# Kernel tuning notes

Measured on AMD Instinct MI355X. Metric: run time of the kernel, lower is better.

The kernel has to match this reference:

```python
import jax, jax.numpy as jnp
import numpy as np

B, T, N, H = 16, 49, 64, 128  # batch, input_window_size-1, nbones, hidden_size


def setup_inputs() -> dict:
    key = jax.random.key(0)
    ks = jax.random.split(key, 13)
    s = 0.1  # keep gate preactivations in a sane range
    inp = {
        "h": jax.random.normal(ks[0], (B, T, N, H), jnp.float32),
        "c_h": jax.random.normal(ks[1], (B, T, N, H), jnp.float32),
        "p": jax.random.normal(ks[2], (B, T, N, H), jnp.float32),
        "g_t": jax.random.normal(ks[3], (B, T, 1, H), jnp.float32),
        "c_g_t": jax.random.normal(ks[4], (B, T, 1, H), jnp.float32),
        # 8 h-update gates stacked: order = (i, f_lt, f_ft, f_rt, f_s, g, o, c)
        "U": jax.random.normal(ks[5], (8, T, H, H), jnp.float32) * s,     # acts on p
        "Wt": jax.random.normal(ks[6], (8, T, 3 * H, H), jnp.float32) * s,  # acts on [h_before,h,h_after]
        "Ws": jax.random.normal(ks[7], (8, T, H, H), jnp.float32) * s,    # acts on h_s_before
        "Zt": jax.random.normal(ks[8], (8, T, H, H), jnp.float32) * s,    # acts on g_t
        "b": jax.random.normal(ks[9], (8, T, 1, H), jnp.float32) * s,
        # 3 g_t-update gates stacked: order = (forget_f, g, o)
        "Wg": jax.random.normal(ks[10], (3, T, H, H), jnp.float32) * s,
        "Zg": jax.random.normal(ks[11], (3, T, H, H), jnp.float32) * s,
        "bg": jax.random.normal(ks[12], (3, T, 1, H), jnp.float32) * s,
        "train": 0,
    }
    return inp


def _forward(h, c_h, p, g_t, c_g_t, U, Wt, Ws, Zt, b, Wg, Zg, bg):
    zt = jnp.zeros_like(h[:, :1])        # temporal padding [B,1,N,H]
    zs = jnp.zeros_like(h[:, :, :1])     # spatial  padding [B,T,1,H]
    h_tb = jnp.concatenate([zt, h[:, :-1]], axis=1)
    h_ta = jnp.concatenate([h[:, 1:], zt], axis=1)
    h_tba = jnp.concatenate([h_tb, h, h_ta], axis=3)   # [B,T,N,3H]
    c_tb = jnp.concatenate([zt, c_h[:, :-1]], axis=1)
    c_ta = jnp.concatenate([c_h[:, 1:], zt], axis=1)
    h_sb = jnp.concatenate([zs, h[:, :, :-1]], axis=2)
    c_sb = jnp.concatenate([zs, c_h[:, :, :-1]], axis=2)

    # all 8 gate preactivations at once; per-timestep weights contracted with einsum
    pre = (jnp.einsum('btnh,gthk->gbtnk', p, U)
           + jnp.einsum('btnd,gtdk->gbtnk', h_tba, Wt)
           + jnp.einsum('btnh,gthk->gbtnk', h_sb, Ws)
           + jnp.einsum('btoh,gthk->gbtok', g_t, Zt)   # o == 1, broadcasts over bones
           + b[:, None])                               # [8,B,T,N,H]
    i_n, f_lt, f_ft, f_rt, f_s, g_n, o_n = jax.nn.sigmoid(pre[:7])
    c_n = jnp.tanh(pre[7])

    c_h_new = (i_n * c_n + f_lt * c_tb + f_ft * c_h + f_rt * c_ta
               + f_s * c_sb + g_n * c_g_t)
    h_new = o_n * jnp.tanh(c_h_new)

    # global (g_t) state update
    h_mean = jnp.mean(h_new, axis=2, keepdims=True)    # [B,T,1,H]
    f_gtf = jax.nn.sigmoid(jnp.einsum('btnh,thk->btnk', h_new, Wg[0])
                           + jnp.einsum('btoh,thk->btok', g_t, Zg[0]) + bg[0])
    g_gtg = jax.nn.sigmoid(jnp.einsum('btoh,thk->btok', h_mean, Wg[1])
                           + jnp.einsum('btoh,thk->btok', g_t, Zg[1]) + bg[1])
    o_gto = jax.nn.sigmoid(jnp.einsum('btoh,thk->btok', h_mean, Wg[2])
                           + jnp.einsum('btoh,thk->btok', g_t, Zg[2]) + bg[2])
    c_g_new = jnp.mean(f_gtf * c_h_new, axis=2, keepdims=True) + g_gtg * c_g_t
    g_new = jnp.tanh(c_g_new) * o_gto
    return h_new, c_h_new, g_new, c_g_new


def reference(h, c_h, p, g_t, c_g_t, U, Wt, Ws, Zt, b, Wg, Zg, bg, train):
    return _forward(h, c_h, p, g_t, c_g_t, U, Wt, Ws, Zt, b, Wg, Zg, bg)
```

## Files before the change

kernel.cpp:

```cpp
#include <hip/hip_runtime.h>
#include <hip/hip_bf16.h>

#define TD 49
#define BD 16
#define ND 64
#define HD 128

typedef float  f32x4  __attribute__((ext_vector_type(4)));
typedef __bf16 bf16x8 __attribute__((ext_vector_type(8)));
typedef __bf16 bf16x4 __attribute__((ext_vector_type(4)));

#define WP_OFF   0u
#define WP_ELEMS 38535168u
#define HB_OFF   38535168u
#define ACT_ELEMS 6422528u
#define PB_OFF   44957696u
#define GB_OFF   51380224u
#define GT_ELEMS 100352u
#define ZP_OFF   51480576u

#define OUT_H    0
#define OUT_CH   6422528
#define OUT_G    12845056
#define OUT_CG   12945408

#define KPAD 136
#define LDS1_BYTES 65536

__device__ __forceinline__ float sigf(float x) {
    return 1.0f / (1.0f + exp2f(-1.442695041f * x));
}
__device__ __forceinline__ float tanhf_fast(float x) {
    x = fminf(fmaxf(x, -20.f), 20.f);
    float e = exp2f(2.885390082f * x);
    return (e - 1.f) / (e + 1.f);
}
__device__ __forceinline__ void gload16(const void* g, void* l) {
    __builtin_amdgcn_global_load_lds((const __attribute__((address_space(1))) void*)g,
                                     (__attribute__((address_space(3))) void*)l, 16, 0, 0);
}

__global__ void prep_acts(const float* __restrict__ h, const float* __restrict__ p,
                          const float* __restrict__ g, __bf16* __restrict__ ws)
{
    unsigned i = blockIdx.x * 256u + threadIdx.x;
    const unsigned HU = ACT_ELEMS / 4u, GU = GT_ELEMS / 4u;
    const float* src;
    unsigned dst;
    if (i < HU)                 { src = h + (size_t)i * 4;          dst = HB_OFF + i * 4; }
    else if (i < 2u*HU)         { unsigned j = i - HU;   src = p + (size_t)j * 4; dst = PB_OFF + j * 4; }
    else if (i < 2u*HU + GU)    { unsigned j = i - 2u*HU; src = g + (size_t)j * 4; dst = GB_OFF + j * 4; }
    else if (i < 2u*HU + GU + 512u) {
        unsigned j = i - 2u*HU - GU;
        bf16x4 z = {};
        *(bf16x4*)(ws + ZP_OFF + j * 4) = z;
        return;
    } else return;
    f32x4 v = *(const f32x4*)src;
    bf16x4 w;
    w[0] = (__bf16)v[0]; w[1] = (__bf16)v[1]; w[2] = (__bf16)v[2]; w[3] = (__bf16)v[3];
    *(bf16x4*)(ws + dst) = w;
}

__global__ __launch_bounds__(256) void prep_w(
    const float* __restrict__ U, const float* __restrict__ Wt,
    const float* __restrict__ Ws, const float* __restrict__ Zt,
    __bf16* __restrict__ wp)
{
    __shared__ __bf16 tile[64 * 132];
    int bid = blockIdx.x;
    int tg  = bid / 12;
    int c   = bid % 12;
    int t   = tg >> 3, g = tg & 7;
    int gt  = g * TD + t;
    int tid = threadIdx.x;
    int k0  = c * 64;

#pragma unroll
    for (int u = 0; u < 8; ++u) {
        int unit = u * 256 + tid;
        int kk = unit >> 5;
        int h4 = (unit & 31) << 2;
        int k  = k0 + kk;
        const float* src;
        if (k < 128)      src = U  + ((size_t)(gt * 128 + k)       << 7);
        else if (k < 512) src = Wt + ((size_t)(gt * 384 + (k-128)) << 7);
        else if (k < 640) src = Ws + ((size_t)(gt * 128 + (k-512)) << 7);
        else              src = Zt + ((size_t)(gt * 128 + (k-640)) << 7);
        f32x4 v = *(const f32x4*)(src + h4);
        bf16x4 w;
        w[0] = (__bf16)v[0]; w[1] = (__bf16)v[1]; w[2] = (__bf16)v[2]; w[3] = (__bf16)v[3];
        *(bf16x4*)(tile + kk * 132 + h4) = w;
    }
    __syncthreads();
#pragma unroll
    for (int u = 0; u < 2; ++u) {
        int unit = u * 256 + tid;
        int hh = unit >> 2;
        int kg = unit & 3;
        bf16x8 v0, v1;
#pragma unroll
        for (int j = 0; j < 8; ++j) v0[j] = tile[(kg * 16 + j) * 132 + hh];
#pragma unroll
        for (int j = 0; j < 8; ++j) v1[j] = tile[(kg * 16 + 8 + j) * 132 + hh];
        __bf16* dst = wp + (size_t)(tg * 128 + hh) * 768 + k0 + kg * 16;
        *(bf16x8*)dst       = v0;
        *(bf16x8*)(dst + 8) = v1;
    }
}

__global__ __launch_bounds__(256, 2) void phase1_kernel(
    const __bf16* __restrict__ ws,
    const float* __restrict__ c_h, const float* __restrict__ c_g_t,
    const float* __restrict__ bias, float* __restrict__ out)
{
    extern __shared__ __bf16 smem[];
    const __bf16* hb = ws + HB_OFF;
    const __bf16* pb = ws + PB_OFF;
    const __bf16* gb = ws + GB_OFF;
    const __bf16* wp = ws + WP_OFF;
    const __bf16* zp = ws + ZP_OFF;

    int bid = blockIdx.x;
    int swz = (bid & 7) * 392 + (bid >> 3);
    int t     = swz >> 6;
    int rem   = swz & 63;
    int mtile = rem >> 3, ntile = rem & 7;

    int tid  = threadIdx.x;
    int wave = tid >> 6, lane = tid & 63;
    int lg = lane >> 4, l16 = lane & 15;

    const int ls   = lane >> 3;
    const int k16s = ((lane & 7) ^ ls) << 3;

    f32x4 acc[2][8];
    const f32x4 vzero = {0.f, 0.f, 0.f, 0.f};
#pragma unroll
    for (int mi = 0; mi < 2; ++mi)
#pragma unroll
        for (int g = 0; g < 8; ++g) acc[mi][g] = vzero;

    int rbA[2], rsA[2], rbB[8], rsB[8];
#pragma unroll
    for (int mi = 0; mi < 2; ++mi) {
        int row = wave * 32 + mi * 16 + l16;
        rbA[mi] = row << 7;
        rsA[mi] = (row & 7) << 4;
    }
#pragma unroll
    for (int g = 0; g < 8; ++g) {
        int row = g * 16 + l16;
        rbB[g] = row << 7;
        rsB[g] = (l16 & 7) << 4;
    }
    const int kb0 = lg << 4;

#define STAGE(BUF, KS) do {                                                     \
        int s_   = (KS) >> 1;                                                   \
        int koff = (((KS) & 1) << 6) + k16s;                                    \
        _Pragma("unroll")                                                       \
        for (int it = 0; it < 4; ++it) {                                        \
            int chunk = it * 4 + wave;                                          \
            int R   = chunk * 8 + ls;                                           \
            int b_  = mtile * 2 + (R >> 6);                                     \
            int n_  = R & 63;                                                   \
            int bt_ = b_ * TD + t;                                              \
            const __bf16* srcA;                                                 \
            if (s_ == 0)      srcA = pb + ((bt_ * ND + n_) << 7) + koff;        \
            else if (s_ == 1) srcA = (t > 0)    ? hb + (((bt_-1) * ND + n_) << 7) + koff : zp; \
            else if (s_ == 2) srcA = hb + ((bt_ * ND + n_) << 7) + koff;        \
            else if (s_ == 3) srcA = (t < TD-1) ? hb + (((bt_+1) * ND + n_) << 7) + koff : zp; \
            else if (s_ == 4) srcA = (n_ > 0)   ? hb + ((bt_ * ND + n_ - 1) << 7) + koff : zp; \
            else              srcA = gb + (bt_ << 7) + koff;                    \
            gload16(srcA, smem + (BUF) * 8192 + chunk * 512);                   \
            int g_ = R >> 4, hc = R & 15;                                       \
            const __bf16* srcB = wp + (size_t)((t * 8 + g_) * 128 + ntile * 16 + hc) * 768 \
                                    + ((KS) << 6) + k16s;                       \
            gload16(srcB, smem + 16384 + (BUF) * 8192 + chunk * 512);           \
        }                                                                       \
    } while (0)

    STAGE(0, 0);
    __syncthreads();

    int buf = 0;
    for (int ks = 0; ks < 12; ++ks) {
        if (ks < 11) STAGE(buf ^ 1, ks + 1);
        const char* Ab = (const char*)(smem + buf * 8192);
        const char* Bb = (const char*)(smem + 16384 + buf * 8192);
#pragma unroll
        for (int ks32 = 0; ks32 < 2; ++ks32) {
            bf16x8 af[2], bfr[8];
#pragma unroll
            for (int mi = 0; mi < 2; ++mi)
                af[mi] = *(const bf16x8*)(Ab + rbA[mi] + (((ks32 << 6) + kb0) ^ rsA[mi]));
#pragma unroll
            for (int g = 0; g < 8; ++g)
                bfr[g] = *(const bf16x8*)(Bb + rbB[g] + (((ks32 << 6) + kb0) ^ rsB[g]));
#pragma unroll
            for (int mi = 0; mi < 2; ++mi)
#pragma unroll
                for (int g = 0; g < 8; ++g)
                    acc[mi][g] = __builtin_amdgcn_mfma_f32_16x16x32_bf16(af[mi], bfr[g], acc[mi][g], 0, 0, 0);
        }
        __syncthreads();
        buf ^= 1;
    }

    const int hcol = ntile * 16 + l16;
    float bv[8];
#pragma unroll
    for (int g = 0; g < 8; ++g) bv[g] = bias[(g * TD + t) * HD + hcol];

#pragma unroll
    for (int mi = 0; mi < 2; ++mi) {
#pragma unroll
        for (int r = 0; r < 4; ++r) {
            int RG = mtile * 128 + wave * 32 + mi * 16 + lg * 4 + r;
            int b  = RG >> 6, nn = RG & 63;
            int bt = b * TD + t;
            int base = ((bt * ND + nn) << 7) + hcol;
            float pre[8];
#pragma unroll
            for (int g = 0; g < 8; ++g) pre[g] = acc[mi][g][r] + bv[g];
            float i_  = sigf(pre[0]);
            float flt = sigf(pre[1]);
            float fft = sigf(pre[2]);
            float frt = sigf(pre[3]);
            float fs  = sigf(pre[4]);
            float gn  = sigf(pre[5]);
            float on  = sigf(pre[6]);
            float cn  = tanhf_fast(pre[7]);
            float ccur = c_h[base];
            float ctb  = (t > 0)      ? c_h[base - ND * HD] : 0.f;
            float cta  = (t < TD - 1) ? c_h[base + ND * HD] : 0.f;
            float csb  = (nn > 0)     ? c_h[base - HD]      : 0.f;
            float cg   = c_g_t[(bt << 7) + hcol];
            float cnew = i_ * cn + flt * ctb + fft * ccur + frt * cta + fs * csb + gn * cg;
            float hnew = on * tanhf_fast(cnew);
            out[OUT_H  + base] = hnew;
            out[OUT_CH + base] = cnew;
        }
    }
#undef STAGE
}

__global__ __launch_bounds__(256, 2) void phase2_kernel(
    const float* __restrict__ g_t, const float* __restrict__ c_g_t,
    const float* __restrict__ Wg,  const float* __restrict__ Zg,
    const float* __restrict__ bg,  float* __restrict__ out)
{
    __shared__ __bf16 A2[64 * KPAD];
    __shared__ __bf16 Wb[128 * KPAD];
    __shared__ float  gts[128];
    __shared__ float  hm[128];
    __shared__ float  dots[5][128];
    __shared__ float  ps[2][128];
    __shared__ float  red[4][128];

    const int bid  = blockIdx.x;
    const int t    = bid >> 4;
    const int b    = bid & 15;
    const int tid  = threadIdx.x;
    const int wv   = tid >> 6;
    const int lane = tid & 63;
    const int lg   = lane >> 4;
    const int l16  = lane & 15;
    const int bt   = b * TD + t;

    const float* hn  = out + OUT_H;
    const float* chn = out + OUT_CH;

#pragma unroll
    for (int j = 0; j < 8; ++j) {
        int fid = j * 256 + tid;
        int r   = fid >> 5;
        int k   = (fid & 31) << 2;
        f32x4 v = *(const f32x4*)(hn + ((bt * ND + r) << 7) + k);
        bf16x4 w;
        w[0] = (__bf16)v[0]; w[1] = (__bf16)v[1]; w[2] = (__bf16)v[2]; w[3] = (__bf16)v[3];
        *(bf16x4*)(A2 + r * KPAD + k) = w;
    }
    if (tid < 128) gts[tid] = g_t[(bt << 7) + tid];
    __syncthreads();

    {
        int c = tid & 127, half = tid >> 7;
        float sum_ = 0.f;
        for (int r2 = 0; r2 < 32; ++r2) sum_ += (float)A2[(half * 32 + r2) * KPAD + c];
        ps[half][c] = sum_;
    }
    __syncthreads();
    if (tid < 128) hm[tid] = (ps[0][tid] + ps[1][tid]) * (1.f / 64.f);

    for (int m = 0; m < 5; ++m) {
        const float* M = (m < 3) ? (Zg + ((size_t)(m * TD + t) << 14))
                                 : (Wg + ((size_t)((m - 2) * TD + t) << 14));
        const bool use_hm = (m >= 3);
        __syncthreads();
#pragma unroll
        for (int j = 0; j < 16; ++j) {
            int fid = j * 256 + tid;
            int k   = fid >> 5;
            int c4  = (fid & 31) << 2;
            f32x4 v = *(const f32x4*)(M + (k << 7) + c4);
            bf16x4 w;
            w[0] = (__bf16)v[0]; w[1] = (__bf16)v[1]; w[2] = (__bf16)v[2]; w[3] = (__bf16)v[3];
            *(bf16x4*)(Wb + (k << 7) + c4) = w;
        }
        __syncthreads();
        {
            int c = tid & 127, half = tid >> 7;
            const float* vec = use_hm ? hm : gts;
            float sum_ = 0.f;
            for (int k = half * 64; k < half * 64 + 64; ++k)
                sum_ += vec[k] * (float)Wb[(k << 7) + c];
            ps[half][c] = sum_;
        }
        __syncthreads();
        if (tid < 128) dots[m][tid] = ps[0][tid] + ps[1][tid];
    }

    {
        const float* M = Wg + ((size_t)t << 14);
        __syncthreads();
#pragma unroll
        for (int j = 0; j < 16; ++j) {
            int fid = j * 256 + tid;
            int k   = fid >> 5;
            int q   = fid & 31;
            f32x4 v = *(const f32x4*)(M + (k << 7) + q * 4);
            int cb = q * 4;
            Wb[(cb + 0) * KPAD + k] = (__bf16)v[0];
            Wb[(cb + 1) * KPAD + k] = (__bf16)v[1];
            Wb[(cb + 2) * KPAD + k] = (__bf16)v[2];
            Wb[(cb + 3) * KPAD + k] = (__bf16)v[3];
        }
        __syncthreads();
    }

    f32x4 acc[8];
    const f32x4 vzero = {0.f, 0.f, 0.f, 0.f};
#pragma unroll
    for (int cf = 0; cf < 8; ++cf) acc[cf] = vzero;
#pragma unroll
    for (int ks = 0; ks < 4; ++ks) {
        int kb = ks * 32 + lg * 8;
        bf16x8 a = *(const bf16x8*)(A2 + (wv * 16 + l16) * KPAD + kb);
#pragma unroll
        for (int cf = 0; cf < 8; ++cf) {
            bf16x8 bfr = *(const bf16x8*)(Wb + (cf * 16 + l16) * KPAD + kb);
            acc[cf] = __builtin_amdgcn_mfma_f32_16x16x32_bf16(a, bfr, acc[cf], 0, 0, 0);
        }
    }

#pragma unroll
    for (int cf = 0; cf < 8; ++cf) {
        int col = cf * 16 + l16;
        float z = dots[0][col] + bg[(0 * TD + t) * HD + col];
        float macc = 0.f;
#pragma unroll
        for (int r = 0; r < 4; ++r) {
            int row = wv * 16 + lg * 4 + r;
            float f  = sigf(acc[cf][r] + z);
            float cv = chn[((bt * ND + row) << 7) + col];
            macc += f * cv;
        }
        macc += __shfl_xor(macc, 16, 64);
        macc += __shfl_xor(macc, 32, 64);
        if (lane < 16) red[wv][col] = macc;
    }
    __syncthreads();
    if (tid < 128) {
        int c = tid;
        float Mn  = (red[0][c] + red[1][c] + red[2][c] + red[3][c]) * (1.f / 64.f);
        float g_g = sigf(dots[3][c] + dots[1][c] + bg[(1 * TD + t) * HD + c]);
        float o_g = sigf(dots[4][c] + dots[2][c] + bg[(2 * TD + t) * HD + c]);
        float cgt = c_g_t[(bt << 7) + c];
        float cgn = Mn + g_g * cgt;
        float gnw = tanhf_fast(cgn) * o_g;
        out[OUT_G  + (bt << 7) + c] = gnw;
        out[OUT_CG + (bt << 7) + c] = cgn;
    }
}

extern "C" void kernel_launch(void* const* d_in, const int* in_sizes, int n_in,
                              void* d_out, int out_size, void* d_ws, size_t ws_size,
                              hipStream_t stream) {
    const float* h     = (const float*)d_in[0];
    const float* c_h   = (const float*)d_in[1];
    const float* p     = (const float*)d_in[2];
    const float* g_t   = (const float*)d_in[3];
    const float* c_g_t = (const float*)d_in[4];
    const float* U     = (const float*)d_in[5];
    const float* Wt    = (const float*)d_in[6];
    const float* Ws    = (const float*)d_in[7];
    const float* Zt    = (const float*)d_in[8];
    const float* b     = (const float*)d_in[9];
    const float* Wg    = (const float*)d_in[10];
    const float* Zg    = (const float*)d_in[11];
    const float* bg    = (const float*)d_in[12];
    float* out = (float*)d_out;
    __bf16* ws = (__bf16*)d_ws;

    prep_acts<<<12644, 256, 0, stream>>>(h, p, g_t, ws);
    prep_w<<<TD * 8 * 12, 256, 0, stream>>>(U, Wt, Ws, Zt, ws + WP_OFF);

    (void)hipFuncSetAttribute(reinterpret_cast<const void*>(phase1_kernel),
                              hipFuncAttributeMaxDynamicSharedMemorySize, LDS1_BYTES);
    phase1_kernel<<<TD * 64, 256, LDS1_BYTES, stream>>>(ws, c_h, c_g_t, b, out);
    phase2_kernel<<<TD * BD, 256, 0, stream>>>(g_t, c_g_t, Wg, Zg, bg, out);
}
```

Measured before the change: 253.3 us.

## Deepen phase1 GEMM pipeline to 4-stage ring and batch four batches per phase2 block

Phase1's K loop changes from a double-buffered 12-step loop over 128-wide K slices to a 24-step loop over 32-wide slices. It uses a 4-slot LDS ring with three slices in flight, precomputed source pointers and explicit vmcnt waits, so global-to-LDS loads overlap the MFMA work better. Phase2 now handles four batches per block (196 blocks instead of 784), so each Zg/Wg weight matrix is converted to bf16 and staged once per four batches instead of once per batch. The costs are more LDS per block, lower occupancy (launch bounds 1) and fewer blocks for the GPU to spread phase2 across.

Result: faster. 234.9 us (-7.3%).

```diff
diff --git a/kernel.cpp b/kernel.cpp
--- a/kernel.cpp
+++ b/kernel.cpp
@@ -11,7 +11,6 @@
 typedef __bf16 bf16x4 __attribute__((ext_vector_type(4)));
 
 #define WP_OFF   0u
-#define WP_ELEMS 38535168u
 #define HB_OFF   38535168u
 #define ACT_ELEMS 6422528u
 #define PB_OFF   44957696u
@@ -26,6 +25,7 @@
 
 #define KPAD 136
 #define LDS1_BYTES 65536
+#define LDS2_BYTES 118784
 
 __device__ __forceinline__ float sigf(float x) {
     return 1.0f / (1.0f + exp2f(-1.442695041f * x));
@@ -131,8 +131,39 @@
     int wave = tid >> 6, lane = tid & 63;
     int lg = lane >> 4, l16 = lane & 15;
 
-    const int ls   = lane >> 3;
-    const int k16s = ((lane & 7) ^ ls) << 3;
+    const __bf16* pA[2][6];
+    const __bf16* pB[2];
+    int dstA[2], dstB[2];
+#pragma unroll
+    for (int it = 0; it < 2; ++it) {
+        int chunk = it * 256 + tid;
+        int row   = chunk >> 2;
+        int k16   = chunk & 3;
+        int ke    = (k16 ^ ((row >> 1) & 3)) * 8;
+        int b_ = mtile * 2 + (row >> 6), n_ = row & 63, bt_ = b_ * TD + t;
+        pA[it][0] = pb + ((bt_ * ND + n_) << 7) + ke;
+        pA[it][1] = (t > 0)      ? hb + (((bt_ - 1) * ND + n_) << 7) + ke : zp + ke;
+        pA[it][2] = hb + ((bt_ * ND + n_) << 7) + ke;
+        pA[it][3] = (t < TD - 1) ? hb + (((bt_ + 1) * ND + n_) << 7) + ke : zp + ke;
+        pA[it][4] = (n_ > 0)     ? hb + ((bt_ * ND + n_ - 1) << 7) + ke : zp + ke;
+        pA[it][5] = gb + (bt_ << 7) + ke;
+        int g_ = row >> 4, hc = row & 15;
+        pB[it] = wp + (size_t)((t * 8 + g_) * 128 + ntile * 16 + hc) * 768 + ke;
+        dstA[it] = chunk * 8;
+        dstB[it] = 16384 + chunk * 8;
+    }
+
+    int rbA[2], rbB[8];
+#pragma unroll
+    for (int mi = 0; mi < 2; ++mi) {
+        int row = wave * 32 + mi * 16 + l16;
+        rbA[mi] = row * 64 + ((lg ^ ((row >> 1) & 3)) << 4);
+    }
+#pragma unroll
+    for (int g = 0; g < 8; ++g) {
+        int row = g * 16 + l16;
+        rbB[g] = 32768 + row * 64 + ((lg ^ ((row >> 1) & 3)) << 4);
+    }
 
     f32x4 acc[2][8];
     const f32x4 vzero = {0.f, 0.f, 0.f, 0.f};
@@ -141,72 +172,43 @@
 #pragma unroll
         for (int g = 0; g < 8; ++g) acc[mi][g] = vzero;
 
-    int rbA[2], rsA[2], rbB[8], rsB[8];
-#pragma unroll
-    for (int mi = 0; mi < 2; ++mi) {
-        int row = wave * 32 + mi * 16 + l16;
-        rbA[mi] = row << 7;
-        rsA[mi] = (row & 7) << 4;
-    }
-#pragma unroll
-    for (int g = 0; g < 8; ++g) {
-        int row = g * 16 + l16;
-        rbB[g] = row << 7;
-        rsB[g] = (l16 & 7) << 4;
-    }
-    const int kb0 = lg << 4;
-
-#define STAGE(BUF, KS) do {                                                     \
-        int s_   = (KS) >> 1;                                                   \
-        int koff = (((KS) & 1) << 6) + k16s;                                    \
+#define STAGE(KS) do {                                                          \
         _Pragma("unroll")                                                       \
-        for (int it = 0; it < 4; ++it) {                                        \
-            int chunk = it * 4 + wave;                                          \
-            int R   = chunk * 8 + ls;                                           \
-            int b_  = mtile * 2 + (R >> 6);                                     \
-            int n_  = R & 63;                                                   \
-            int bt_ = b_ * TD + t;                                              \
-            const __bf16* srcA;                                                 \
-            if (s_ == 0)      srcA = pb + ((bt_ * ND + n_) << 7) + koff;        \
-            else if (s_ == 1) srcA = (t > 0)    ? hb + (((bt_-1) * ND + n_) << 7) + koff : zp; \
-            else if (s_ == 2) srcA = hb + ((bt_ * ND + n_) << 7) + koff;        \
-            else if (s_ == 3) srcA = (t < TD-1) ? hb + (((bt_+1) * ND + n_) << 7) + koff : zp; \
-            else if (s_ == 4) srcA = (n_ > 0)   ? hb + ((bt_ * ND + n_ - 1) << 7) + koff : zp; \
-            else              srcA = gb + (bt_ << 7) + koff;                    \
-            gload16(srcA, smem + (BUF) * 8192 + chunk * 512);                   \
-            int g_ = R >> 4, hc = R & 15;                                       \
-            const __bf16* srcB = wp + (size_t)((t * 8 + g_) * 128 + ntile * 16 + hc) * 768 \
-                                    + ((KS) << 6) + k16s;                       \
-            gload16(srcB, smem + 16384 + (BUF) * 8192 + chunk * 512);           \
+        for (int it = 0; it < 2; ++it) {                                        \
+            gload16(pA[it][(KS) >> 2] + ((KS) & 3) * 32,                        \
+                    smem + ((KS) & 3) * 4096 + dstA[it]);                       \
+            gload16(pB[it] + (KS) * 32,                                         \
+                    smem + ((KS) & 3) * 4096 + dstB[it]);                       \
         }                                                                       \
     } while (0)
 
-    STAGE(0, 0);
-    __syncthreads();
-
-    int buf = 0;
-    for (int ks = 0; ks < 12; ++ks) {
-        if (ks < 11) STAGE(buf ^ 1, ks + 1);
-        const char* Ab = (const char*)(smem + buf * 8192);
-        const char* Bb = (const char*)(smem + 16384 + buf * 8192);
-#pragma unroll
-        for (int ks32 = 0; ks32 < 2; ++ks32) {
-            bf16x8 af[2], bfr[8];
-#pragma unroll
-            for (int mi = 0; mi < 2; ++mi)
-                af[mi] = *(const bf16x8*)(Ab + rbA[mi] + (((ks32 << 6) + kb0) ^ rsA[mi]));
-#pragma unroll
-            for (int g = 0; g < 8; ++g)
-                bfr[g] = *(const bf16x8*)(Bb + rbB[g] + (((ks32 << 6) + kb0) ^ rsB[g]));
-#pragma unroll
-            for (int mi = 0; mi < 2; ++mi)
-#pragma unroll
-                for (int g = 0; g < 8; ++g)
-                    acc[mi][g] = __builtin_amdgcn_mfma_f32_16x16x32_bf16(af[mi], bfr[g], acc[mi][g], 0, 0, 0);
-        }
-        __syncthreads();
-        buf ^= 1;
-    }
+    STAGE(0); STAGE(1); STAGE(2);
+    asm volatile("s_waitcnt vmcnt(8)" ::: "memory");
+    __builtin_amdgcn_s_barrier();
+
+#pragma unroll
+    for (int ks = 0; ks < 24; ++ks) {
+        if (ks + 3 < 24) STAGE(ks + 3);
+        const char* base = (const char*)smem + (ks & 3) * 8192;
+        bf16x8 af[2], bfr[8];
+        af[0] = *(const bf16x8*)(base + rbA[0]);
+        af[1] = *(const bf16x8*)(base + rbA[1]);
+#pragma unroll
+        for (int g = 0; g < 8; ++g)
+            bfr[g] = *(const bf16x8*)(base + rbB[g]);
+#pragma unroll
+        for (int g = 0; g < 8; ++g) {
+            acc[0][g] = __builtin_amdgcn_mfma_f32_16x16x32_bf16(af[0], bfr[g], acc[0][g], 0, 0, 0);
+            acc[1][g] = __builtin_amdgcn_mfma_f32_16x16x32_bf16(af[1], bfr[g], acc[1][g], 0, 0, 0);
+        }
+        if (ks < 23) {
+            if (ks < 21)       asm volatile("s_waitcnt vmcnt(8)" ::: "memory");
+            else if (ks == 21) asm volatile("s_waitcnt vmcnt(4)" ::: "memory");
+            else               asm volatile("s_waitcnt vmcnt(0)" ::: "memory");
+            __builtin_amdgcn_s_barrier();
+        }
+    }
+#undef STAGE
 
     const int hcol = ntile * 16 + l16;
     float bv[8];
@@ -243,93 +245,87 @@
             out[OUT_CH + base] = cnew;
         }
     }
-#undef STAGE
-}
-
-__global__ __launch_bounds__(256, 2) void phase2_kernel(
+}
+
+__global__ __launch_bounds__(256, 1) void phase2_kernel(
     const float* __restrict__ g_t, const float* __restrict__ c_g_t,
     const float* __restrict__ Wg,  const float* __restrict__ Zg,
     const float* __restrict__ bg,  float* __restrict__ out)
 {
-    __shared__ __bf16 A2[64 * KPAD];
-    __shared__ __bf16 Wb[128 * KPAD];
-    __shared__ float  gts[128];
-    __shared__ float  hm[128];
-    __shared__ float  dots[5][128];
-    __shared__ float  ps[2][128];
-    __shared__ float  red[4][128];
-
-    const int bid  = blockIdx.x;
-    const int t    = bid >> 4;
-    const int b    = bid & 15;
-    const int tid  = threadIdx.x;
-    const int wv   = tid >> 6;
-    const int lane = tid & 63;
-    const int lg   = lane >> 4;
-    const int l16  = lane & 15;
-    const int bt   = b * TD + t;
+    extern __shared__ char sm2[];
+    __bf16* A2  = (__bf16*)sm2;
+    __bf16* Wb  = (__bf16*)(sm2 + 69632);
+    float*  gts = (float*)(sm2 + 69632 + 34816);
+    float*  hm  = (float*)(sm2 + 69632 + 34816 + 2048);
+    float*  dts = (float*)(sm2 + 69632 + 34816 + 4096);
+
+    int bid = blockIdx.x;
+    int t = bid >> 2, bq = bid & 3;
+    int tid = threadIdx.x;
+    int wv = tid >> 6, lane = tid & 63, lg = lane >> 4, l16 = lane & 15;
 
     const float* hn  = out + OUT_H;
     const float* chn = out + OUT_CH;
 
 #pragma unroll
-    for (int j = 0; j < 8; ++j) {
+    for (int j = 0; j < 32; ++j) {
         int fid = j * 256 + tid;
-        int r   = fid >> 5;
-        int k   = (fid & 31) << 2;
-        f32x4 v = *(const f32x4*)(hn + ((bt * ND + r) << 7) + k);
+        int r = fid >> 5, k = (fid & 31) << 2;
+        int b = bq * 4 + (r >> 6), n = r & 63, bt = b * TD + t;
+        f32x4 v = *(const f32x4*)(hn + ((bt * ND + n) << 7) + k);
         bf16x4 w;
         w[0] = (__bf16)v[0]; w[1] = (__bf16)v[1]; w[2] = (__bf16)v[2]; w[3] = (__bf16)v[3];
         *(bf16x4*)(A2 + r * KPAD + k) = w;
     }
-    if (tid < 128) gts[tid] = g_t[(bt << 7) + tid];
+#pragma unroll
+    for (int j = 0; j < 2; ++j) {
+        int idx = j * 256 + tid;
+        int b4 = idx >> 7, c = idx & 127;
+        gts[idx] = g_t[(((bq * 4 + b4) * TD + t) << 7) + c];
+    }
     __syncthreads();
 
-    {
-        int c = tid & 127, half = tid >> 7;
-        float sum_ = 0.f;
-        for (int r2 = 0; r2 < 32; ++r2) sum_ += (float)A2[(half * 32 + r2) * KPAD + c];
-        ps[half][c] = sum_;
+#pragma unroll
+    for (int j = 0; j < 2; ++j) {
+        int idx = j * 256 + tid;
+        int b4 = idx >> 7, c = idx & 127;
+        float s = 0.f;
+        for (int n = 0; n < 64; ++n) s += (float)A2[(b4 * 64 + n) * KPAD + c];
+        hm[idx] = s * (1.f / 64.f);
     }
     __syncthreads();
-    if (tid < 128) hm[tid] = (ps[0][tid] + ps[1][tid]) * (1.f / 64.f);
 
     for (int m = 0; m < 5; ++m) {
         const float* M = (m < 3) ? (Zg + ((size_t)(m * TD + t) << 14))
                                  : (Wg + ((size_t)((m - 2) * TD + t) << 14));
-        const bool use_hm = (m >= 3);
-        __syncthreads();
 #pragma unroll
         for (int j = 0; j < 16; ++j) {
             int fid = j * 256 + tid;
-            int k   = fid >> 5;
-            int c4  = (fid & 31) << 2;
+            int k = fid >> 5, c4 = (fid & 31) << 2;
             f32x4 v = *(const f32x4*)(M + (k << 7) + c4);
             bf16x4 w;
             w[0] = (__bf16)v[0]; w[1] = (__bf16)v[1]; w[2] = (__bf16)v[2]; w[3] = (__bf16)v[3];
-            *(bf16x4*)(Wb + (k << 7) + c4) = w;
+            *(bf16x4*)(Wb + k * KPAD + c4) = w;
         }
         __syncthreads();
-        {
-            int c = tid & 127, half = tid >> 7;
-            const float* vec = use_hm ? hm : gts;
-            float sum_ = 0.f;
-            for (int k = half * 64; k < half * 64 + 64; ++k)
-                sum_ += vec[k] * (float)Wb[(k << 7) + c];
-            ps[half][c] = sum_;
+        const float* vec = (m >= 3) ? hm : gts;
+#pragma unroll
+        for (int j = 0; j < 2; ++j) {
+            int idx = j * 256 + tid;
+            int b4 = idx >> 7, c = idx & 127;
+            float s = 0.f;
+            for (int k = 0; k < 128; ++k) s += vec[b4 * 128 + k] * (float)Wb[k * KPAD + c];
+            dts[(m * 4 + b4) * 128 + c] = s;
         }
         __syncthreads();
-        if (tid < 128) dots[m][tid] = ps[0][tid] + ps[1][tid];
     }
 
     {
         const float* M = Wg + ((size_t)t << 14);
-        __syncthreads();
 #pragma unroll
         for (int j = 0; j < 16; ++j) {
             int fid = j * 256 + tid;
-            int k   = fid >> 5;
-            int q   = fid & 31;
+            int k = fid >> 5, q = fid & 31;
             f32x4 v = *(const f32x4*)(M + (k << 7) + q * 4);
             int cb = q * 4;
             Wb[(cb + 0) * KPAD + k] = (__bf16)v[0];
@@ -340,48 +336,57 @@
         __syncthreads();
     }
 
-    f32x4 acc[8];
+    f32x4 acc[4][8];
     const f32x4 vzero = {0.f, 0.f, 0.f, 0.f};
 #pragma unroll
-    for (int cf = 0; cf < 8; ++cf) acc[cf] = vzero;
+    for (int mi = 0; mi < 4; ++mi)
+#pragma unroll
+        for (int ni = 0; ni < 8; ++ni) acc[mi][ni] = vzero;
 #pragma unroll
     for (int ks = 0; ks < 4; ++ks) {
         int kb = ks * 32 + lg * 8;
-        bf16x8 a = *(const bf16x8*)(A2 + (wv * 16 + l16) * KPAD + kb);
-#pragma unroll
-        for (int cf = 0; cf < 8; ++cf) {
-            bf16x8 bfr = *(const bf16x8*)(Wb + (cf * 16 + l16) * KPAD + kb);
-            acc[cf] = __builtin_amdgcn_mfma_f32_16x16x32_bf16(a, bfr, acc[cf], 0, 0, 0);
-        }
-    }
-
-#pragma unroll
-    for (int cf = 0; cf < 8; ++cf) {
-        int col = cf * 16 + l16;
-        float z = dots[0][col] + bg[(0 * TD + t) * HD + col];
+        bf16x8 a[4];
+#pragma unroll
+        for (int mi = 0; mi < 4; ++mi)
+            a[mi] = *(const bf16x8*)(A2 + (wv * 64 + mi * 16 + l16) * KPAD + kb);
+#pragma unroll
+        for (int ni = 0; ni < 8; ++ni) {
+            bf16x8 bfr = *(const bf16x8*)(Wb + (ni * 16 + l16) * KPAD + kb);
+#pragma unroll
+            for (int mi = 0; mi < 4; ++mi)
+                acc[mi][ni] = __builtin_amdgcn_mfma_f32_16x16x32_bf16(a[mi], bfr, acc[mi][ni], 0, 0, 0);
+        }
+    }
+
+    int b = bq * 4 + wv, bt = b * TD + t;
+#pragma unroll
+    for (int ni = 0; ni < 8; ++ni) {
+        int col = ni * 16 + l16;
+        float z = dts[(0 * 4 + wv) * 128 + col] + bg[t * HD + col];
         float macc = 0.f;
 #pragma unroll
-        for (int r = 0; r < 4; ++r) {
-            int row = wv * 16 + lg * 4 + r;
-            float f  = sigf(acc[cf][r] + z);
-            float cv = chn[((bt * ND + row) << 7) + col];
-            macc += f * cv;
+        for (int mi = 0; mi < 4; ++mi) {
+#pragma unroll
+            for (int r = 0; r < 4; ++r) {
+                int row = mi * 16 + lg * 4 + r;
+                float f  = sigf(acc[mi][ni][r] + z);
+                float cv = chn[((bt * ND + row) << 7) + col];
+                macc += f * cv;
+            }
         }
         macc += __shfl_xor(macc, 16, 64);
         macc += __shfl_xor(macc, 32, 64);
-        if (lane < 16) red[wv][col] = macc;
-    }
-    __syncthreads();
-    if (tid < 128) {
-        int c = tid;
-        float Mn  = (red[0][c] + red[1][c] + red[2][c] + red[3][c]) * (1.f / 64.f);
-        float g_g = sigf(dots[3][c] + dots[1][c] + bg[(1 * TD + t) * HD + c]);
-        float o_g = sigf(dots[4][c] + dots[2][c] + bg[(2 * TD + t) * HD + c]);
-        float cgt = c_g_t[(bt << 7) + c];
-        float cgn = Mn + g_g * cgt;
-        float gnw = tanhf_fast(cgn) * o_g;
-        out[OUT_G  + (bt << 7) + c] = gnw;
-        out[OUT_CG + (bt << 7) + c] = cgn;
+        if (lg == 0) {
+            float Mn  = macc * (1.f / 64.f);
+            float g_g = sigf(dts[(3 * 4 + wv) * 128 + col] + dts[(1 * 4 + wv) * 128 + col]
+                             + bg[(TD + t) * HD + col]);
+            float o_g = sigf(dts[(4 * 4 + wv) * 128 + col] + dts[(2 * 4 + wv) * 128 + col]
+                             + bg[(2 * TD + t) * HD + col]);
+            float cgt = c_g_t[(bt << 7) + col];
+            float cgn = Mn + g_g * cgt;
+            out[OUT_G  + (bt << 7) + col] = tanhf_fast(cgn) * o_g;
+            out[OUT_CG + (bt << 7) + col] = cgn;
+        }
     }
 }
 
@@ -409,6 +414,8 @@
 
     (void)hipFuncSetAttribute(reinterpret_cast<const void*>(phase1_kernel),
                               hipFuncAttributeMaxDynamicSharedMemorySize, LDS1_BYTES);
+    (void)hipFuncSetAttribute(reinterpret_cast<const void*>(phase2_kernel),
+                              hipFuncAttributeMaxDynamicSharedMemorySize, LDS2_BYTES);
     phase1_kernel<<<TD * 64, 256, LDS1_BYTES, stream>>>(ws, c_h, c_g_t, b, out);
-    phase2_kernel<<<TD * BD, 256, 0, stream>>>(g_t, c_g_t, Wg, Zg, bg, out);
-}
+    phase2_kernel<<<TD * 4, 256, LDS2_BYTES, stream>>>(g_t, c_g_t, Wg, Zg, bg, out);
+}
```
